# Kernel tuning notes

Measured on AMD Instinct MI355X. Metric: run time of the kernel, lower is better.

Reference implementation:

```python
import jax, jax.numpy as jnp
import numpy as np
from jax import lax

B = 16384
BN_EPS = 1e-5


def setup_inputs() -> dict:
    key = jax.random.key(0)
    ks = jax.random.split(key, 6)
    x = jax.random.normal(ks[0], (B, 1, 28, 28), jnp.float32)
    conv_w = jax.random.normal(ks[1], (4, 1, 3, 3), jnp.float32) * 0.2
    bn_gamma = jnp.ones((4,), jnp.float32)
    bn_beta = jnp.zeros((4,), jnp.float32)
    bn_mean = jnp.zeros((4,), jnp.float32)
    bn_var = jnp.ones((4,), jnp.float32)
    var_params = jax.random.normal(ks[2], (4,), jnp.float32)
    lin_w = jax.random.normal(ks[3], (10, 784), jnp.float32) * 0.03
    lin_b = jnp.zeros((10,), jnp.float32)
    return {"x": x, "conv_w": conv_w, "bn_gamma": bn_gamma, "bn_beta": bn_beta,
            "bn_mean": bn_mean, "bn_var": bn_var, "var_params": var_params,
            "lin_w": lin_w, "lin_b": lin_b}


def _ry_w0(s, theta):
    # apply RY(theta) to wire 0 (axis -2) of real state s[..., 2, 2]
    c, si = jnp.cos(theta * 0.5), jnp.sin(theta * 0.5)
    R = jnp.stack([jnp.stack([c, -si]), jnp.stack([si, c])])
    return jnp.einsum('ij,...jk->...ik', R, s)


def _ry_w1(s, theta):
    # apply RY(theta) to wire 1 (axis -1)
    c, si = jnp.cos(theta * 0.5), jnp.sin(theta * 0.5)
    R = jnp.stack([jnp.stack([c, -si]), jnp.stack([si, c])])
    return jnp.einsum('ij,...kj->...ki', R, s)


def _quantum_features(img, v):
    # img: [B, 28, 28] -> features [B, 196*4] (patch-major, 4 expvals each)
    b = img.shape[0]
    p = img.reshape(b, 14, 2, 14, 2).transpose(0, 1, 3, 2, 4)  # [B,14,14,2,2]
    # encoding RYs on same wire compose: angles a = p0+p2 (wire0), b = p1+p3 (wire1)
    ha = (p[..., 0, 0] + p[..., 1, 0]) * 0.5
    hb = (p[..., 0, 1] + p[..., 1, 1]) * 0.5
    w0 = jnp.stack([jnp.cos(ha), jnp.sin(ha)], axis=-1)
    w1 = jnp.stack([jnp.cos(hb), jnp.sin(hb)], axis=-1)
    s = w0[..., :, None] * w1[..., None, :]  # real statevector [B,14,14,2,2]
    # CNOT(control=0, target=1): flip wire1 where wire0 == 1
    s = jnp.stack([s[..., 0, :], s[..., 1, ::-1]], axis=-2)
    s = _ry_w0(s, v[0])
    s = _ry_w1(s, v[1])
    # CNOT(control=1, target=0): flip wire0 where wire1 == 1
    s = jnp.stack([s[..., :, 0], s[..., ::-1, 1]], axis=-1)
    s = _ry_w0(s, v[2])
    s = _ry_w1(s, v[3])
    z0 = jnp.sum(s[..., 0, :] ** 2 - s[..., 1, :] ** 2, axis=-1)
    z1 = jnp.sum(s[..., :, 0] ** 2 - s[..., :, 1] ** 2, axis=-1)
    x0 = 2.0 * jnp.sum(s[..., 0, :] * s[..., 1, :], axis=-1)
    x1 = 2.0 * jnp.sum(s[..., :, 0] * s[..., :, 1], axis=-1)
    return jnp.stack([z0, z1, x0, x1], axis=-1).reshape(b, -1)  # [B,784]


def reference(x, conv_w, bn_gamma, bn_beta, bn_mean, bn_var, var_params, lin_w, lin_b):
    b = x.shape[0]
    # classical branch: conv(s=2,p=1) -> BN (eval) -> ReLU -> flatten
    h = lax.conv_general_dilated(x, conv_w, window_strides=(2, 2),
                                 padding=((1, 1), (1, 1)))  # [B,4,14,14]
    inv = bn_gamma / jnp.sqrt(bn_var + BN_EPS)
    h = h * inv[None, :, None, None] + (bn_beta - bn_mean * inv)[None, :, None, None]
    h = jnp.maximum(h, 0.0)
    cls_out = h.reshape(b, -1)  # [B,784]
    # quantum branch over 2x2 patches
    q_out = _quantum_features(x[:, 0], var_params)  # [B,784]
    fused = cls_out + q_out
    logits = fused @ lin_w.T + lin_b
    return jax.nn.log_softmax(logits, axis=-1)
```

## Files before the change

### kernel.cpp

```cpp
#include <hip/hip_runtime.h>
#include <math.h>


#define NW 4
#define SCLS_STRIDE 794

typedef __fp16 h2 __attribute__((ext_vector_type(2)));
typedef __fp16 h4 __attribute__((ext_vector_type(4)));

#define FDOT2(a, b, c) __builtin_amdgcn_fdot2((a), (b), (c), false)
#define PK(a, b) __builtin_amdgcn_cvt_pkrtz((a), (b))

__device__ __forceinline__ unsigned h2u(h2 v) { return __builtin_bit_cast(unsigned, v); }
__device__ __forceinline__ h2 uh2(unsigned v) { return __builtin_bit_cast(h2, v); }

__device__ __forceinline__ float2 red32x2(float x) {
    int v;
    v = __builtin_amdgcn_update_dpp(0, __float_as_int(x), 0x111, 0xf, 0xf, true); x += __int_as_float(v);
    v = __builtin_amdgcn_update_dpp(0, __float_as_int(x), 0x112, 0xf, 0xf, true); x += __int_as_float(v);
    v = __builtin_amdgcn_update_dpp(0, __float_as_int(x), 0x114, 0xf, 0xf, true); x += __int_as_float(v);
    v = __builtin_amdgcn_update_dpp(0, __float_as_int(x), 0x118, 0xf, 0xf, true); x += __int_as_float(v);
    v = __builtin_amdgcn_update_dpp(0, __float_as_int(x), 0x142, 0xa, 0xf, true); x += __int_as_float(v);
    float2 r;
    r.x = __int_as_float(__builtin_amdgcn_readlane(__float_as_int(x), 31));
    r.y = __int_as_float(__builtin_amdgcn_readlane(__float_as_int(x), 63));
    return r;
}

__device__ __forceinline__ void load_patch(const float* __restrict__ xs,
                                           unsigned i, int j, float* a) {
    int omid = (int)(2 * i) * 28 + 2 * j;
    float2 Rm = *(const float2*)(xs + omid);
    float2 Rb = *(const float2*)(xs + omid + 28);
    int ot = omid - 28; ot = (ot > 0) ? ot : 0;
    float2 Rt = *(const float2*)(xs + ot);
    int olt = omid - 30; olt = (olt > 0) ? olt : 0;
    float2 Lt = *(const float2*)(xs + olt);
    int olm = omid - 2; olm = (olm > 0) ? olm : 0;
    float2 Lm = *(const float2*)(xs + olm);
    float2 Lb = *(const float2*)(xs + olm + 28);
    float mt = (i > 0) ? 1.f : 0.f;
    float ml = (j > 0) ? 1.f : 0.f;
    a[0] = Lt.y * (mt * ml); a[1] = Rt.x * mt; a[2] = Rt.y * mt;
    a[3] = Lm.y * ml;        a[4] = Rm.x;      a[5] = Rm.y;
    a[6] = Lb.y * ml;        a[7] = Rb.x;      a[8] = Rb.y;
}

__global__ __launch_bounds__(256, 4)
void quanv_fused(const float* __restrict__ x,
                 const float* __restrict__ conv_w,
                 const float* __restrict__ bn_gamma,
                 const float* __restrict__ bn_beta,
                 const float* __restrict__ bn_mean,
                 const float* __restrict__ bn_var,
                 const float* __restrict__ var_params,
                 const float* __restrict__ lin_w,
                 const float* __restrict__ lin_b,
                 float* __restrict__ out, int B)
{
    __shared__ __align__(16) __fp16 lwh[7840];
    __shared__ __align__(16) __fp16 sclsAll[NW * 2 * SCLS_STRIDE];

    const int tid  = threadIdx.x;
    const int wave = tid >> 6;
    const int lane = tid & 63;
    const int half = lane >> 5;
    const int l32  = lane & 31;

    const int s  = blockIdx.x * (NW * 2) + wave * 2 + half;
    const int sc = (s < B) ? s : (B - 1);
    const float* xs = x + (size_t)sc * 784;
    __fp16* myscls = &sclsAll[(wave * 2 + half) * SCLS_STRIDE];

    {
        const float4* src = (const float4*)lin_w;
        #pragma unroll
        for (int t = 0; t < 8; ++t) {
            int i = tid + t * 256;
            if (i < 1960) {
                float4 v = src[i];
                h2 a = PK(v.x, v.y);
                h2 b = PK(v.z, v.w);
                h4 w4 = { a.x, a.y, b.x, b.y };
                *(h4*)&lwh[4 * i] = w4;
            }
        }
    }

    h2 w2[36];
    h2 addc2[4];
    #pragma unroll
    for (int c = 0; c < 4; ++c) {
        float iv = bn_gamma[c] * rsqrtf(bn_var[c] + 1e-5f);
        float ac = bn_beta[c] - bn_mean[c] * iv;
        addc2[c] = PK(ac, ac);
        #pragma unroll
        for (int k = 0; k < 9; ++k) {
            float wf = conv_w[c * 9 + k] * iv;
            w2[c * 9 + k] = PK(wf, wf);
        }
    }
    h2 cv2[4], sv2[4];
    #pragma unroll
    for (int k = 0; k < 4; ++k) {
        float sk, ck;
        __sincosf(var_params[k] * 0.5f, &sk, &ck);
        cv2[k] = PK(ck, ck);
        sv2[k] = PK(sk, sk);
    }

    h2 qh[7][2];
    #pragma unroll
    for (int tt = 0; tt < 4; ++tt) {
        const int tA = 2 * tt, tB = 2 * tt + 1;
        int pA = l32 + 32 * tA, pB = l32 + 32 * tB;
        bool actA = (pA < 196), actB = (pB < 196);
        int pcA = actA ? pA : 195, pcB = actB ? pB : 195;
        unsigned iA = (unsigned)pcA / 14u; int jA = pcA - (int)iA * 14;
        unsigned iB = (unsigned)pcB / 14u; int jB = pcB - (int)iB * 14;

        float aA[9], aB[9];
        load_patch(xs, iA, jA, aA);
        load_patch(xs, iB, jB, aB);

        h2 apk[9];
        #pragma unroll
        for (int k = 0; k < 9; ++k) apk[k] = PK(aA[k], aB[k]);
        const h2 hz = { (__fp16)0.f, (__fp16)0.f };
        #pragma unroll
        for (int c = 0; c < 4; ++c) {
            h2 acc = addc2[c];
            #pragma unroll
            for (int k = 0; k < 9; ++k) acc += w2[c * 9 + k] * apk[k];
            acc = __builtin_elementwise_max(acc, hz);
            if (actA) myscls[c * 196 + pcA] = acc.x;
            if (actB) myscls[c * 196 + pcB] = acc.y;
        }

        float haA = 0.5f * (aA[4] + aA[7]), hbA = 0.5f * (aA[5] + aA[8]);
        float haB = 0.5f * (aB[4] + aB[7]), hbB = 0.5f * (aB[5] + aB[8]);
        float c0A, s0A, c1A, s1A, c0B, s0B, c1B, s1B;
        __sincosf(haA, &s0A, &c0A); __sincosf(hbA, &s1A, &c1A);
        __sincosf(haB, &s0B, &c0B); __sincosf(hbB, &s1B, &c1B);
        h2 M00 = PK(c0A * c1A, c0B * c1B);
        h2 M01 = PK(c0A * s1A, c0B * s1B);
        h2 M10 = PK(s0A * s1A, s0B * s1B);
        h2 M11 = PK(s0A * c1A, s0B * c1B);
        h2 T00 = cv2[0] * M00 - sv2[0] * M10;
        h2 T01 = cv2[0] * M01 - sv2[0] * M11;
        h2 T10 = sv2[0] * M00 + cv2[0] * M10;
        h2 T11 = sv2[0] * M01 + cv2[0] * M11;
        h2 U00 = cv2[1] * T00 - sv2[1] * T01;
        h2 U01 = sv2[1] * T00 + cv2[1] * T01;
        h2 U10 = cv2[1] * T10 - sv2[1] * T11;
        h2 U11 = sv2[1] * T10 + cv2[1] * T11;
        h2 V01 = U11, V11 = U01;
        h2 P00 = cv2[2] * U00 - sv2[2] * U10;
        h2 P01 = cv2[2] * V01 - sv2[2] * V11;
        h2 P10 = sv2[2] * U00 + cv2[2] * U10;
        h2 P11 = sv2[2] * V01 + cv2[2] * V11;
        h2 Q00 = cv2[3] * P00 - sv2[3] * P01;
        h2 Q01 = sv2[3] * P00 + cv2[3] * P01;
        h2 Q10 = cv2[3] * P10 - sv2[3] * P11;
        h2 Q11 = sv2[3] * P10 + cv2[3] * P11;
        h2 sq00 = Q00 * Q00, sq01 = Q01 * Q01, sq10 = Q10 * Q10, sq11 = Q11 * Q11;
        h2 z0 = (sq00 + sq01) - (sq10 + sq11);
        h2 z1 = (sq00 + sq10) - (sq01 + sq11);
        h2 x0 = Q00 * Q10 + Q01 * Q11; x0 = x0 + x0;
        h2 x1 = Q00 * Q01 + Q10 * Q11; x1 = x1 + x1;

        unsigned z0u = h2u(z0), z1u = h2u(z1), x0u = h2u(x0), x1u = h2u(x1);
        qh[tA][0] = uh2(__builtin_amdgcn_perm(z1u, z0u, 0x05040100));
        qh[tA][1] = uh2(__builtin_amdgcn_perm(x1u, x0u, 0x05040100));
        if (tB < 7) {
            qh[tB][0] = uh2(__builtin_amdgcn_perm(z1u, z0u, 0x07060302));
            qh[tB][1] = uh2(__builtin_amdgcn_perm(x1u, x0u, 0x07060302));
        }
    }

    __syncthreads();

    float ps[10];
    #pragma unroll
    for (int o = 0; o < 10; ++o) ps[o] = 0.f;

    const h2 hz = { (__fp16)0.f, (__fp16)0.f };
    #pragma unroll
    for (int t = 0; t < 7; ++t) {
        int p = l32 + 32 * t;
        bool act = (p < 196);
        int pc = act ? p : 195;
        h2 c0 = *(const h2*)&myscls[4 * pc];
        h2 c1 = *(const h2*)&myscls[4 * pc + 2];
        h2 f0 = c0 + qh[t][0];
        h2 f1 = c1 + qh[t][1];
        f0 = act ? f0 : hz;
        f1 = act ? f1 : hz;
        const __fp16* wbase = &lwh[4 * pc];
        #pragma unroll
        for (int o = 0; o < 10; ++o) {
            h4 wv = *(const h4*)&wbase[o * 784];
            h2 wlo = __builtin_shufflevector(wv, wv, 0, 1);
            h2 whi = __builtin_shufflevector(wv, wv, 2, 3);
            ps[o] = FDOT2(f0, wlo, ps[o]);
            ps[o] = FDOT2(f1, whi, ps[o]);
        }
    }

    float lg[10];
    #pragma unroll
    for (int o = 0; o < 10; ++o) {
        float2 r = red32x2(ps[o]);
        lg[o] = (half ? r.y : r.x) + lin_b[o];
    }

    float mx = lg[0];
    #pragma unroll
    for (int o = 1; o < 10; ++o) mx = fmaxf(mx, lg[o]);
    float se = 0.f;
    #pragma unroll
    for (int o = 0; o < 10; ++o) se += __expf(lg[o] - mx);
    float ls = __logf(se);

    if (l32 < 10 && s < B) {
        float v = lg[0];
        #pragma unroll
        for (int o = 1; o < 10; ++o) v = (l32 == o) ? lg[o] : v;
        out[(size_t)s * 10 + l32] = v - mx - ls;
    }
}

extern "C" void kernel_launch(void* const* d_in, const int* in_sizes, int n_in,
                              void* d_out, int out_size, void* d_ws, size_t ws_size,
                              hipStream_t stream) {
    const float* x          = (const float*)d_in[0];
    const float* conv_w     = (const float*)d_in[1];
    const float* bn_gamma   = (const float*)d_in[2];
    const float* bn_beta    = (const float*)d_in[3];
    const float* bn_mean    = (const float*)d_in[4];
    const float* bn_var     = (const float*)d_in[5];
    const float* var_params = (const float*)d_in[6];
    const float* lin_w      = (const float*)d_in[7];
    const float* lin_b      = (const float*)d_in[8];
    float* out = (float*)d_out;

    const int B = in_sizes[0] / 784;
    const int blocks = (B + NW * 2 - 1) / (NW * 2);
    quanv_fused<<<blocks, 256, 0, stream>>>(x, conv_w, bn_gamma, bn_beta, bn_mean,
                                            bn_var, var_params, lin_w, lin_b, out, B);
}
```

Before: 111.7 us.

## Precompute fp16 linear weights in a separate kernel and read them from global memory

Adds a small pre-kernel that converts lin_w to fp16 in the workspace once per call. The main kernel no longer stages the full weight matrix into LDS per block, so the per-block conversion work and about 15 KB of shared memory go away. Weights are instead read directly from global/L2 in the dot-product loop. The block-wide barrier is replaced by a wave-local LDS waitcnt, and the launch-bounds occupancy hint rises from 4 to 6 blocks. This adds a second kernel launch and relies on cache hits for the repeated weight reads, and the bare waitcnt assumes each wave only reads the scratch data it wrote itself.

```diff
diff --git a/kernel.cpp b/kernel.cpp
--- a/kernel.cpp
+++ b/kernel.cpp
@@ -46,7 +46,18 @@
     a[6] = Lb.y * ml;        a[7] = Rb.x;      a[8] = Rb.y;
 }
 
-__global__ __launch_bounds__(256, 4)
+__global__ void w_to_f16(const float* __restrict__ lin_w, __fp16* __restrict__ w16) {
+    int i = blockIdx.x * 256 + threadIdx.x;
+    if (i < 1960) {
+        float4 v = ((const float4*)lin_w)[i];
+        h2 a = PK(v.x, v.y);
+        h2 b = PK(v.z, v.w);
+        h4 w4 = { a.x, a.y, b.x, b.y };
+        *(h4*)&w16[4 * i] = w4;
+    }
+}
+
+__global__ __launch_bounds__(256, 6)
 void quanv_fused(const float* __restrict__ x,
                  const float* __restrict__ conv_w,
                  const float* __restrict__ bn_gamma,
@@ -54,11 +65,10 @@
                  const float* __restrict__ bn_mean,
                  const float* __restrict__ bn_var,
                  const float* __restrict__ var_params,
-                 const float* __restrict__ lin_w,
+                 const __fp16* __restrict__ w16,
                  const float* __restrict__ lin_b,
                  float* __restrict__ out, int B)
 {
-    __shared__ __align__(16) __fp16 lwh[7840];
     __shared__ __align__(16) __fp16 sclsAll[NW * 2 * SCLS_STRIDE];
 
     const int tid  = threadIdx.x;
@@ -71,21 +81,6 @@
     const int sc = (s < B) ? s : (B - 1);
     const float* xs = x + (size_t)sc * 784;
     __fp16* myscls = &sclsAll[(wave * 2 + half) * SCLS_STRIDE];
-
-    {
-        const float4* src = (const float4*)lin_w;
-        #pragma unroll
-        for (int t = 0; t < 8; ++t) {
-            int i = tid + t * 256;
-            if (i < 1960) {
-                float4 v = src[i];
-                h2 a = PK(v.x, v.y);
-                h2 b = PK(v.z, v.w);
-                h4 w4 = { a.x, a.y, b.x, b.y };
-                *(h4*)&lwh[4 * i] = w4;
-            }
-        }
-    }
 
     h2 w2[36];
     h2 addc2[4];
@@ -178,28 +173,29 @@
         }
     }
 
-    __syncthreads();
+    asm volatile("s_waitcnt lgkmcnt(0)" ::: "memory");
 
     float ps[10];
     #pragma unroll
     for (int o = 0; o < 10; ++o) ps[o] = 0.f;
 
+    const h4* gw = (const h4*)w16;
     const h2 hz = { (__fp16)0.f, (__fp16)0.f };
     #pragma unroll
     for (int t = 0; t < 7; ++t) {
         int p = l32 + 32 * t;
         bool act = (p < 196);
         int pc = act ? p : 195;
-        h2 c0 = *(const h2*)&myscls[4 * pc];
-        h2 c1 = *(const h2*)&myscls[4 * pc + 2];
+        h4 cl4 = *(const h4*)&myscls[4 * pc];
+        h2 c0 = __builtin_shufflevector(cl4, cl4, 0, 1);
+        h2 c1 = __builtin_shufflevector(cl4, cl4, 2, 3);
         h2 f0 = c0 + qh[t][0];
         h2 f1 = c1 + qh[t][1];
         f0 = act ? f0 : hz;
         f1 = act ? f1 : hz;
-        const __fp16* wbase = &lwh[4 * pc];
         #pragma unroll
         for (int o = 0; o < 10; ++o) {
-            h4 wv = *(const h4*)&wbase[o * 784];
+            h4 wv = gw[o * 196 + pc];
             h2 wlo = __builtin_shufflevector(wv, wv, 0, 1);
             h2 whi = __builtin_shufflevector(wv, wv, 2, 3);
             ps[o] = FDOT2(f0, wlo, ps[o]);
@@ -243,9 +239,13 @@
     const float* lin_w      = (const float*)d_in[7];
     const float* lin_b      = (const float*)d_in[8];
     float* out = (float*)d_out;
+    __fp16* w16 = (__fp16*)d_ws;
 
     const int B = in_sizes[0] / 784;
+
+    w_to_f16<<<8, 256, 0, stream>>>(lin_w, w16);
+
     const int blocks = (B + NW * 2 - 1) / (NW * 2);
     quanv_fused<<<blocks, 256, 0, stream>>>(x, conv_w, bn_gamma, bn_beta, bn_mean,
-                                            bn_var, var_params, lin_w, lin_b, out, B);
-}
+                                            bn_var, var_params, w16, lin_b, out, B);
+}
```

Result: slower. 151.8 us (+35.9%).
